# Kernel tuning notes

Measured on AMD Instinct MI355X. Metric: run time of the kernel, lower is better.

The kernel has to match this reference:

```python
import jax, jax.numpy as jnp
import numpy as np
from jax import lax

N_P = 0.5      # module_cfg.n_p
CUTOFF = 0.3   # module_cfg.cutoff


def setup_inputs() -> dict:
    key = jax.random.key(0)
    k1, k2, k3, k4 = jax.random.split(key, 4)
    h = jax.random.normal(k1, (1, 8192, 256), jnp.float32)
    pos = jax.random.normal(k2, (8192, 3), jnp.float32)
    W = jax.random.normal(k3, (256, 256), jnp.float32) / 16.0  # ~ Linear init scale
    b = jax.random.normal(k4, (256,), jnp.float32) * 0.01
    return {"h": h, "pos": pos, "W": W, "b": b}


def fps_indices(pos, k, select=0):
    """Farthest point sampling; returns the k selected indices in ascending
    index order (matching torch boolean-mask indexing pos[selected])."""
    n = pos.shape[0]
    selected = jnp.zeros(n, dtype=bool).at[select].set(True)
    d = jnp.linalg.norm(pos - pos[select], axis=-1)  # (N,) euclidean, as torch.pairwise_distance
    d = jnp.where(selected, -jnp.inf, d)

    def body(i, carry):
        sel, dist = carry
        new = jnp.argmax(dist)
        sel = sel.at[new].set(True)
        dist = jnp.minimum(dist, jnp.linalg.norm(pos - pos[new], axis=-1))
        dist = jnp.where(sel, -jnp.inf, dist)
        return sel, dist

    sel, _ = lax.fori_loop(0, k - 1, body, (selected, d))
    return jnp.nonzero(sel, size=k)[0]  # exactly k True entries, sorted


def reference(h, pos, W, b):
    B, num_res, c_s = h.shape
    n_nodes = int(num_res * N_P)  # num_res * n_p // 1

    idx = fps_indices(pos, n_nodes)          # (n_nodes,)
    new_node_pos = pos[idx]                  # (n_nodes, 3)

    # torch.cdist(pos, new_node_pos, p=3): Minkowski p=3 distance
    diff = jnp.abs(pos[:, None, :] - new_node_pos[None, :, :])  # (N, n_nodes, 3)
    dist = jnp.cbrt(jnp.sum(diff ** 3, axis=-1))                 # (N, n_nodes)

    # sparse membership mask (fixed-shape equivalent of the nonzero edge list)
    mask = dist < CUTOFF                      # (N, n_nodes) bool

    # sparse gather-matmul: aggregate residue features into each sampled node
    agg = jnp.einsum('nm,bnc->bmc', mask.astype(h.dtype), h)     # (B, n_nodes, c_s)
    new_node_embed = agg @ W.T + b            # nn.Linear(c_s, c_s)
    return new_node_embed, new_node_pos, mask
```

## Files before the change

### kernel.cpp

```cpp
#include <hip/hip_runtime.h>
#include <hip/hip_bf16.h>
#include <cmath>

#define FPS_N 8192
#define FPS_K 4096
#define CS    256
#define FT    1024
#define PPT   8
#define NEGINF (-__builtin_inff())

__device__ __forceinline__ float p3sum(float x, float y, float z,
                                       float nx, float ny, float nz) {
  float dx = fabsf(__fsub_rn(x, nx));
  float dy = fabsf(__fsub_rn(y, ny));
  float dz = fabsf(__fsub_rn(z, nz));
  float cx = __fmul_rn(__fmul_rn(dx, dx), dx);
  float cy = __fmul_rn(__fmul_rn(dy, dy), dy);
  float cz = __fmul_rn(__fmul_rn(dz, dz), dz);
  return __fadd_rn(__fadd_rn(cx, cy), cz);
}

__device__ __forceinline__ float eucl2(float x, float y, float z,
                                       float nx, float ny, float nz) {
  float dx = __fsub_rn(x, nx);
  float dy = __fsub_rn(y, ny);
  float dz = __fsub_rn(z, nz);
  return __fadd_rn(__fadd_rn(__fmul_rn(dx, dx), __fmul_rn(dy, dy)),
                   __fmul_rn(dz, dz));
}

#define LEXGT(va, ka, vb, kb) (((va) > (vb)) || ((va) == (vb) && ((ka) < (kb))))

template<int CTRL>
__device__ __forceinline__ int dppi(int a) {
  return __builtin_amdgcn_update_dpp(a, a, CTRL, 0xF, 0xF, false);
}
template<int CTRL>
__device__ __forceinline__ float dppf(float a) {
  return __int_as_float(__builtin_amdgcn_update_dpp(__float_as_int(a), __float_as_int(a), CTRL, 0xF, 0xF, false));
}

template<int CTRL>
__device__ __forceinline__ void dpp_sel5(float& v, int& k, float& x, float& y, float& z) {
  float pv = dppf<CTRL>(v); int pk = dppi<CTRL>(k);
  float px = dppf<CTRL>(x); float py = dppf<CTRL>(y); float pz = dppf<CTRL>(z);
  bool t = LEXGT(pv, pk, v, k);
  v = t ? pv : v; k = t ? pk : k;
  x = t ? px : x; y = t ? py : y; z = t ? pz : z;
}

template<int CTRL>
__device__ __forceinline__ void dpp_top2(float& v1, int& k1, float& v2, int& k2) {
  float p1 = dppf<CTRL>(v1); int q1 = dppi<CTRL>(k1);
  float p2 = dppf<CTRL>(v2); int q2 = dppi<CTRL>(k2);
  bool t = LEXGT(p1, q1, v1, k1);
  float lv = t ? v1 : p1; int lk = t ? k1 : q1;
  float ov = t ? p2 : v2; int ok = t ? q2 : k2;
  v1 = t ? p1 : v1; k1 = t ? q1 : k1;
  bool u = LEXGT(lv, lk, ov, ok);
  v2 = u ? lv : ov; k2 = u ? lk : ok;
}

#define PAIR2(v1, k1, v2, k2, a, ka, b, kb) { bool t_ = LEXGT(b, kb, a, ka); \
  v1 = t_ ? (b) : (a); k1 = t_ ? (kb) : (ka); v2 = t_ ? (a) : (b); k2 = t_ ? (ka) : (kb); }

#define MERGE22(v1, k1, v2, k2, w1, l1, w2, l2) { \
  bool t_ = LEXGT(w1, l1, v1, k1); \
  float lv_ = t_ ? (v1) : (w1); int lk_ = t_ ? (k1) : (l1); \
  float ov_ = t_ ? (w2) : (v2); int ok_ = t_ ? (l2) : (k2); \
  v1 = t_ ? (w1) : (v1); k1 = t_ ? (l1) : (k1); \
  bool u_ = LEXGT(lv_, lk_, ov_, ok_); \
  v2 = u_ ? lv_ : ov_; k2 = u_ ? lk_ : ok_; }

#define RESCAN2() { \
  float A1, B1, C1, D1, A2, B2, C2, D2; int Ak, Bk, Ck, Dk, Ak2, Bk2, Ck2, Dk2; \
  PAIR2(A1, Ak, A2, Ak2, dd[0], key[0], dd[1], key[1]) \
  PAIR2(B1, Bk, B2, Bk2, dd[2], key[2], dd[3], key[3]) \
  PAIR2(C1, Ck, C2, Ck2, dd[4], key[4], dd[5], key[5]) \
  PAIR2(D1, Dk, D2, Dk2, dd[6], key[6], dd[7], key[7]) \
  MERGE22(A1, Ak, A2, Ak2, B1, Bk, B2, Bk2) \
  MERGE22(C1, Ck, C2, Ck2, D1, Dk, D2, Dk2) \
  MERGE22(A1, Ak, A2, Ak2, C1, Ck, C2, Ck2) \
  bv = A1; bkey = Ak; bv2 = A2; bk2 = Ak2; }

#define WAVE_PUBLISH2(sn) { \
  float rv1 = bv; int rk1 = bkey; float rv2 = bv2; int rk2 = bk2; \
  dpp_top2<0x111>(rv1, rk1, rv2, rk2); dpp_top2<0x112>(rv1, rk1, rv2, rk2); \
  dpp_top2<0x114>(rv1, rk1, rv2, rk2); dpp_top2<0x118>(rv1, rk1, rv2, rk2); \
  dpp_top2<0x142>(rv1, rk1, rv2, rk2); dpp_top2<0x143>(rv1, rk1, rv2, rk2); \
  const int k1u = __builtin_amdgcn_readlane(rk1, 63); \
  const int v2u = __builtin_amdgcn_readlane(__float_as_int(rv2), 63); \
  const int k2u = __builtin_amdgcn_readlane(rk2, 63); \
  int* s_ = &slots[(sn) * 192 + wave * 12]; \
  if (bkey == k1u) { \
    float sx = x[0], sy = y[0], sz = z[0]; \
    _Pragma("unroll") \
    for (int j = 0; j < PPT; ++j) \
      if (j == (bkey & 7)) { sx = x[j]; sy = y[j]; sz = z[j]; } \
    s_[0] = __float_as_int(bv); s_[1] = bkey; \
    s_[2] = __float_as_int(sx); s_[3] = __float_as_int(sy); s_[4] = __float_as_int(sz); \
    if (bk2 == k2u) { \
      float tx = x[0], ty = y[0], tz = z[0]; \
      _Pragma("unroll") \
      for (int j = 0; j < PPT; ++j) \
        if (j == (bk2 & 7)) { tx = x[j]; ty = y[j]; tz = z[j]; } \
      s_[5] = v2u; s_[6] = k2u; \
      s_[7] = __float_as_int(tx); s_[8] = __float_as_int(ty); s_[9] = __float_as_int(tz); \
    } \
  } else if (bkey == k2u) { \
    float sx = x[0], sy = y[0], sz = z[0]; \
    _Pragma("unroll") \
    for (int j = 0; j < PPT; ++j) \
      if (j == (bkey & 7)) { sx = x[j]; sy = y[j]; sz = z[j]; } \
    s_[5] = __float_as_int(bv); s_[6] = bkey; \
    s_[7] = __float_as_int(sx); s_[8] = __float_as_int(sy); s_[9] = __float_as_int(sz); \
  } }

__global__ __launch_bounds__(1024) void bin_kernel(const float* __restrict__ pos,
                                                   float* __restrict__ px,
                                                   float* __restrict__ py,
                                                   float* __restrict__ pz,
                                                   unsigned short* __restrict__ ids16,
                                                   unsigned char* __restrict__ selb) {
  __shared__ int hist[4096];
  __shared__ int part[1024];
  const int tid = threadIdx.x;
#pragma unroll
  for (int i = 0; i < 4; ++i) hist[tid * 4 + i] = 0;
  ((int*)selb)[tid * 2 + 0] = 0;
  ((int*)selb)[tid * 2 + 1] = 0;
  if (tid == 0) selb[0] = 1;
  __syncthreads();

  float qx[8], qy[8], qz[8];
  int cell[8];
  {
    const float4* p4 = (const float4*)pos + tid * 6;
    float4 a0 = p4[0], a1 = p4[1], a2 = p4[2], a3 = p4[3], a4 = p4[4], a5 = p4[5];
    qx[0]=a0.x; qy[0]=a0.y; qz[0]=a0.z;
    qx[1]=a0.w; qy[1]=a1.x; qz[1]=a1.y;
    qx[2]=a1.z; qy[2]=a1.w; qz[2]=a2.x;
    qx[3]=a2.y; qy[3]=a2.z; qz[3]=a2.w;
    qx[4]=a3.x; qy[4]=a3.y; qz[4]=a3.z;
    qx[5]=a3.w; qy[5]=a4.x; qz[5]=a4.y;
    qx[6]=a4.z; qy[6]=a4.w; qz[6]=a5.x;
    qx[7]=a5.y; qy[7]=a5.z; qz[7]=a5.w;
  }
#pragma unroll
  for (int j = 0; j < 8; ++j) {
    int ix = min(max((int)floorf((qx[j] + 4.0f) * 2.0f), 0), 15);
    int iy = min(max((int)floorf((qy[j] + 4.0f) * 2.0f), 0), 15);
    int iz = min(max((int)floorf((qz[j] + 4.0f) * 2.0f), 0), 15);
    int m = 0;
#pragma unroll
    for (int b = 0; b < 4; ++b)
      m |= (((ix >> b) & 1) << (3 * b)) | (((iy >> b) & 1) << (3 * b + 1)) |
           (((iz >> b) & 1) << (3 * b + 2));
    cell[j] = m;
    atomicAdd(&hist[m], 1);
  }
  __syncthreads();
  int h0 = hist[tid*4], h1 = hist[tid*4+1], h2 = hist[tid*4+2], h3 = hist[tid*4+3];
  int s = h0 + h1 + h2 + h3;
  part[tid] = s;
  __syncthreads();
  for (int off = 1; off < 1024; off <<= 1) {
    int u = (tid >= off) ? part[tid - off] : 0;
    __syncthreads();
    part[tid] += u;
    __syncthreads();
  }
  int base = part[tid] - s;
  hist[tid*4+0] = base;
  hist[tid*4+1] = base + h0;
  hist[tid*4+2] = base + h0 + h1;
  hist[tid*4+3] = base + h0 + h1 + h2;
  __syncthreads();
#pragma unroll
  for (int j = 0; j < 8; ++j) {
    int slot = atomicAdd(&hist[cell[j]], 1);
    px[slot] = qx[j];
    py[slot] = qy[j];
    pz[slot] = qz[j];
    ids16[slot] = (unsigned short)(tid * 8 + j);
  }
}

__global__ __launch_bounds__(FT) void fps_kernel(const float* __restrict__ pos,
                                                 const float* __restrict__ spx,
                                                 const float* __restrict__ spy,
                                                 const float* __restrict__ spz,
                                                 const unsigned short* __restrict__ sid,
                                                 unsigned char* __restrict__ selb) {
  __shared__ int slots[2 * 192];
  const int tid = threadIdx.x, lane = tid & 63, wave = tid >> 6;

  float x[PPT], y[PPT], z[PPT], dd[PPT];
  int key[PPT];
  const float p0x = pos[0], p0y = pos[1], p0z = pos[2];
  {
    int4 b0 = ((const int4*)sid)[tid];
    int op[4] = { b0.x, b0.y, b0.z, b0.w };
#pragma unroll
    for (int j = 0; j < PPT; ++j) {
      int oid = (j & 1) ? ((op[j >> 1] >> 16) & 0xffff) : (op[j >> 1] & 0xffff);
      key[j] = (oid << 13) | (tid * PPT + j);
      float X = spx[tid * PPT + j], Y = spy[tid * PPT + j], Z = spz[tid * PPT + j];
      x[j] = X; y[j] = Y; z[j] = Z;
      float s = eucl2(X, Y, Z, p0x, p0y, p0z);
      dd[j] = (oid == 0) ? NEGINF : sqrtf(s);
    }
  }
  float mnx = x[0], mny = y[0], mnz = z[0], mxx = x[0], mxy = y[0], mxz = z[0];
#pragma unroll
  for (int j = 1; j < PPT; ++j) {
    mnx = fminf(mnx, x[j]); mny = fminf(mny, y[j]); mnz = fminf(mnz, z[j]);
    mxx = fmaxf(mxx, x[j]); mxy = fmaxf(mxy, y[j]); mxz = fmaxf(mxz, z[j]);
  }

  unsigned selmask = 0;
  float bv, bv2; int bkey, bk2;
  RESCAN2();
  WAVE_PUBLISH2(0);
  __syncthreads();

  int sel = 0, p = 0;
  while (sel < FPS_K - 1) {
    const int pn = p ^ 1;
    const int row = lane & 15;
    const int4 q0 = *(const int4*)&slots[p * 192 + row * 12 + 0];
    const int4 q1 = *(const int4*)&slots[p * 192 + row * 12 + 4];
    const int4 q2 = *(const int4*)&slots[p * 192 + row * 12 + 8];
    float ev = __int_as_float(q0.x); int ek = q0.y;
    float ex = __int_as_float(q0.z), ey = __int_as_float(q0.w), ez = __int_as_float(q1.x);
    const float sv2 = __int_as_float(q1.y); const int sk2 = q1.z;
    const float sx2 = __int_as_float(q1.w), sy2 = __int_as_float(q2.x), sz2 = __int_as_float(q2.y);
    bool avail2 = true;

    int A = 0;
    bool stop = false, own = false, fire = false;
    const int cap = FPS_K - 1 - sel;
    float a0x=0, a0y=0, a0z=0, a1x=0, a1y=0, a1z=0, a2x=0, a2y=0, a2z=0, a3x=0, a3y=0, a3z=0;

#define PSTEP(AX, AY, AZ, ACCCHK) \
    if (!stop) { \
      float mv = ev; int mk = ek; float mx = ex, my = ey, mz = ez; \
      dpp_sel5<0xB1>(mv, mk, mx, my, mz); \
      dpp_sel5<0x4E>(mv, mk, mx, my, mz); \
      dpp_sel5<0x124>(mv, mk, mx, my, mz); \
      dpp_sel5<0x128>(mv, mk, mx, my, mz); \
      bool ok = true; \
      ACCCHK \
      if (!ok) stop = true; \
      else { \
        AX = mx; AY = my; AZ = mz; \
        const int stor = mk & 8191; \
        if ((stor >> 3) == tid) { \
          const int jj = stor & 7; \
          _Pragma("unroll") \
          for (int j = 0; j < PPT; ++j) if (j == jj) dd[j] = NEGINF; \
          selmask |= (1u << jj); \
          own = true; \
        } \
        const int ww = stor >> 9; \
        if (row == ww) { \
          if (avail2) { ev = sv2; ek = sk2; ex = sx2; ey = sy2; ez = sz2; avail2 = false; } \
          else { ev = NEGINF; ek = 0x7fffffff; } \
        } \
        ++A; \
        if (A >= cap || A >= 4) stop = true; \
      } \
    }

    PSTEP(a0x, a0y, a0z, )
    PSTEP(a1x, a1y, a1z,
      ok = (sqrtf(eucl2(mx, my, mz, a0x, a0y, a0z)) >= mv);)
    PSTEP(a2x, a2y, a2z,
      ok = (sqrtf(eucl2(mx, my, mz, a0x, a0y, a0z)) >= mv)
        && (sqrtf(eucl2(mx, my, mz, a1x, a1y, a1z)) >= mv);)
    PSTEP(a3x, a3y, a3z,
      ok = (sqrtf(eucl2(mx, my, mz, a0x, a0y, a0z)) >= mv)
        && (sqrtf(eucl2(mx, my, mz, a1x, a1y, a1z)) >= mv)
        && (sqrtf(eucl2(mx, my, mz, a2x, a2y, a2z)) >= mv);)
#undef PSTEP

    const float lg = fmaxf(bv, 0.f);
    const float lg2 = lg * lg;
#define UPDC(c, AX, AY, AZ) \
    if ((c) < A) { \
      float cx = fminf(fmaxf(AX, mnx), mxx); \
      float cy = fminf(fmaxf(AY, mny), mxy); \
      float cz = fminf(fmaxf(AZ, mnz), mxz); \
      float ddx = AX - cx, ddy = AY - cy, ddz = AZ - cz; \
      float bd2 = ddx * ddx + ddy * ddy + ddz * ddz; \
      if (bd2 * 0.999f < lg2) { \
        _Pragma("unroll") \
        for (int j = 0; j < PPT; ++j) \
          dd[j] = fminf(dd[j], sqrtf(eucl2(x[j], y[j], z[j], AX, AY, AZ))); \
        fire = true; \
      } \
    }
    UPDC(0, a0x, a0y, a0z)
    UPDC(1, a1x, a1y, a1z)
    UPDC(2, a2x, a2y, a2z)
    UPDC(3, a3x, a3y, a3z)
#undef UPDC

    if (__ballot((fire || own) ? 1 : 0)) {
      if (fire || own) { RESCAN2(); }
      WAVE_PUBLISH2(pn);
    } else {
      if (lane < 12) slots[pn * 192 + wave * 12 + lane] = slots[p * 192 + wave * 12 + lane];
    }
    sel += A;
    p = pn;
    __syncthreads();
  }

#pragma unroll
  for (int j = 0; j < PPT; ++j)
    if ((selmask >> j) & 1) selb[key[j] >> 13] = 1;
}

__global__ __launch_bounds__(1024) void emit_kernel(const unsigned char* __restrict__ selb,
                                                    const float* __restrict__ pos,
                                                    float* __restrict__ pos_out) {
  __shared__ int sc[1024];
  const int tid = threadIdx.x;
  int w0 = ((const int*)selb)[tid * 2 + 0];
  int w1 = ((const int*)selb)[tid * 2 + 1];
  int cnt = __popc(w0) + __popc(w1);
  sc[tid] = cnt;
  __syncthreads();
  for (int off = 1; off < 1024; off <<= 1) {
    int u = (tid >= off) ? sc[tid - off] : 0;
    __syncthreads();
    sc[tid] += u;
    __syncthreads();
  }
  int r = sc[tid] - cnt;
#pragma unroll
  for (int j = 0; j < 8; ++j) {
    int w = (j < 4) ? w0 : w1;
    if ((w >> ((j & 3) * 8)) & 1) {
      int oi = tid * 8 + j;
      pos_out[r * 3 + 0] = pos[oi * 3 + 0];
      pos_out[r * 3 + 1] = pos[oi * 3 + 1];
      pos_out[r * 3 + 2] = pos[oi * 3 + 2];
      ++r;
    }
  }
}

__global__ __launch_bounds__(256) void wt_kernel(const float* __restrict__ W,
                                                 float* __restrict__ WT) {
  int i = blockIdx.x * 256 + threadIdx.x;
  int c = i >> 8, cp = i & 255;
  WT[i] = W[cp * 256 + c];
}

__global__ __launch_bounds__(256) void agg_linear_kernel(
    const float* __restrict__ h, const float* __restrict__ pos,
    const float* __restrict__ nodepos, const float* __restrict__ WT,
    const float* __restrict__ bias, float* __restrict__ embed, float sb) {
  const int m = blockIdx.x;
  const int tid = threadIdx.x;
  const int lane = tid & 63, wave = tid >> 6;
  const float nx = nodepos[m * 3 + 0];
  const float ny = nodepos[m * 3 + 1];
  const float nz = nodepos[m * 3 + 2];
  const float4* h4 = (const float4*)h;

  float4 acc = make_float4(0.f, 0.f, 0.f, 0.f);
  const int base0 = wave * (FPS_N / 4);
  for (int base = base0; base < base0 + (FPS_N / 4); base += 64) {
    int n = base + lane;
    float qx = pos[n * 3 + 0], qy = pos[n * 3 + 1], qz = pos[n * 3 + 2];
    unsigned long long mb = __ballot((p3sum(qx, qy, qz, nx, ny, nz) <= sb) ? 1 : 0);
    while (mb) {
      int b = __ffsll(mb) - 1;
      mb &= (mb - 1);
      float4 hv = h4[(size_t)(base + b) * 64 + lane];
      acc.x += hv.x; acc.y += hv.y; acc.z += hv.z; acc.w += hv.w;
    }
  }

  __shared__ float lacc[4][256];
  lacc[wave][lane * 4 + 0] = acc.x;
  lacc[wave][lane * 4 + 1] = acc.y;
  lacc[wave][lane * 4 + 2] = acc.z;
  lacc[wave][lane * 4 + 3] = acc.w;
  __syncthreads();
  __shared__ float aggrow[256];
  float aggv = ((lacc[0][tid] + lacc[1][tid]) + lacc[2][tid]) + lacc[3][tid];
  aggrow[tid] = aggv;
  __syncthreads();

  float o = bias[tid];
#pragma unroll 8
  for (int c = 0; c < 256; ++c)
    o = fmaf(aggrow[c], WT[c * 256 + tid], o);
  embed[(size_t)m * 256 + tid] = o;
}

__global__ __launch_bounds__(256) void mask_kernel(const float* __restrict__ pos,
                                                   const float* __restrict__ nodepos,
                                                   float* __restrict__ maskout,
                                                   float sb) {
  int n  = blockIdx.y;
  int m0 = (blockIdx.x * 256 + threadIdx.x) * 4;
  float x = pos[n * 3 + 0], y = pos[n * 3 + 1], z = pos[n * 3 + 2];
  const float4* np4 = (const float4*)(nodepos + (size_t)m0 * 3);
  float4 a = np4[0], bq = np4[1], cq = np4[2];
  float4 r;
  r.x = (p3sum(x, y, z, a.x,  a.y,  a.z)  <= sb) ? 1.0f : 0.0f;
  r.y = (p3sum(x, y, z, a.w,  bq.x, bq.y) <= sb) ? 1.0f : 0.0f;
  r.z = (p3sum(x, y, z, bq.z, bq.w, cq.x) <= sb) ? 1.0f : 0.0f;
  r.w = (p3sum(x, y, z, cq.y, cq.z, cq.w) <= sb) ? 1.0f : 0.0f;
  *(float4*)(maskout + (size_t)n * FPS_K + m0) = r;
}

extern "C" void kernel_launch(void* const* d_in, const int* in_sizes, int n_in,
                              void* d_out, int out_size, void* d_ws, size_t ws_size,
                              hipStream_t stream) {
  (void)in_sizes; (void)n_in; (void)out_size; (void)d_ws; (void)ws_size;
  const float* h   = (const float*)d_in[0];
  const float* pos = (const float*)d_in[1];
  const float* W   = (const float*)d_in[2];
  const float* b   = (const float*)d_in[3];

  float* out     = (float*)d_out;
  float* embed   = out;
  float* pos_out = out + (size_t)FPS_K * CS;
  float* mask    = pos_out + (size_t)FPS_K * 3;
  float* WT      = mask;
  float* px      = mask + (1 << 21);
  float* py      = px + FPS_N;
  float* pz      = py + FPS_N;
  unsigned short* ids16 = (unsigned short*)(pz + FPS_N);
  unsigned char*  selb  = ((unsigned char*)ids16) + 2 * FPS_N;

  const float  t    = 0.3f;
  const float  ulpv = nextafterf(t, 1.0f) - t;
  const double rmid = (double)t - (double)ulpv * 0.5;
  const double C    = rmid * rmid * rmid;
  float sb = (float)C;
  if (!((double)sb < C)) sb = nextafterf(sb, 0.0f);

  hipLaunchKernelGGL(bin_kernel, dim3(1), dim3(1024), 0, stream,
                     pos, px, py, pz, ids16, selb);
  hipLaunchKernelGGL(fps_kernel, dim3(1), dim3(FT), 0, stream,
                     pos, px, py, pz, ids16, selb);
  hipLaunchKernelGGL(emit_kernel, dim3(1), dim3(1024), 0, stream,
                     selb, pos, pos_out);
  hipLaunchKernelGGL(wt_kernel, dim3(256), dim3(256), 0, stream, W, WT);
  hipLaunchKernelGGL(agg_linear_kernel, dim3(FPS_K), dim3(256), 0, stream,
                     h, pos, pos_out, WT, b, embed, sb);
  hipLaunchKernelGGL(mask_kernel, dim3(4, FPS_N), dim3(256), 0, stream,
                     pos, pos_out, mask, sb);
}
```

Before: 7.297 ms.

## Replace four-step speculative FPS selection with a single top-2 DPP reduction

The FPS loop used to run up to four sequential 5-value DPP argmax reductions per iteration, accepting up to four points when they were far enough apart. It now runs one DPP top-2 reduction over value and key only, then fetches coordinates from shared slots for the winner and the best second candidate. This cuts per-iteration shuffle and select work and register pressure. The cost is at most two accepted points per barrier-separated iteration, so more outer iterations and __syncthreads calls may be needed.

```diff
diff --git a/kernel.cpp b/kernel.cpp
--- a/kernel.cpp
+++ b/kernel.cpp
@@ -8,6 +8,7 @@
 #define FT    1024
 #define PPT   8
 #define NEGINF (-__builtin_inff())
+#define KMAX  0x7fffffff
 
 __device__ __forceinline__ float p3sum(float x, float y, float z,
                                        float nx, float ny, float nz) {
@@ -38,15 +39,6 @@
 template<int CTRL>
 __device__ __forceinline__ float dppf(float a) {
   return __int_as_float(__builtin_amdgcn_update_dpp(__float_as_int(a), __float_as_int(a), CTRL, 0xF, 0xF, false));
-}
-
-template<int CTRL>
-__device__ __forceinline__ void dpp_sel5(float& v, int& k, float& x, float& y, float& z) {
-  float pv = dppf<CTRL>(v); int pk = dppi<CTRL>(k);
-  float px = dppf<CTRL>(x); float py = dppf<CTRL>(y); float pz = dppf<CTRL>(z);
-  bool t = LEXGT(pv, pk, v, k);
-  v = t ? pv : v; k = t ? pk : k;
-  x = t ? px : x; y = t ? py : y; z = t ? pz : z;
 }
 
 template<int CTRL>
@@ -228,83 +220,81 @@
   while (sel < FPS_K - 1) {
     const int pn = p ^ 1;
     const int row = lane & 15;
-    const int4 q0 = *(const int4*)&slots[p * 192 + row * 12 + 0];
-    const int4 q1 = *(const int4*)&slots[p * 192 + row * 12 + 4];
-    const int4 q2 = *(const int4*)&slots[p * 192 + row * 12 + 8];
-    float ev = __int_as_float(q0.x); int ek = q0.y;
-    float ex = __int_as_float(q0.z), ey = __int_as_float(q0.w), ez = __int_as_float(q1.x);
-    const float sv2 = __int_as_float(q1.y); const int sk2 = q1.z;
-    const float sx2 = __int_as_float(q1.w), sy2 = __int_as_float(q2.x), sz2 = __int_as_float(q2.y);
-    bool avail2 = true;
-
-    int A = 0;
-    bool stop = false, own = false, fire = false;
+    const int2 e1 = *(const int2*)&slots[p * 192 + row * 12];
+    float mv1 = __int_as_float(e1.x); int mk1 = e1.y;
+    float mv2 = NEGINF; int mk2 = KMAX;
+    dpp_top2<0xB1>(mv1, mk1, mv2, mk2);
+    dpp_top2<0x4E>(mv1, mk1, mv2, mk2);
+    dpp_top2<0x124>(mv1, mk1, mv2, mk2);
+    dpp_top2<0x128>(mv1, mk1, mv2, mk2);
+
+    const int stor1 = mk1 & 8191;
+    const int w1w   = stor1 >> 9;
+    const int* r1 = &slots[p * 192 + w1w * 12];
+    const float w1x = __int_as_float(r1[2]);
+    const float w1y = __int_as_float(r1[3]);
+    const float w1z = __int_as_float(r1[4]);
+    const float sv2 = __int_as_float(r1[5]);
+    const int   sk2 = r1[6];
+    const int  w2aw = (mk2 & 8191) >> 9;
+    const int* r2 = &slots[p * 192 + w2aw * 12];
+    const bool bsec = LEXGT(sv2, sk2, mv2, mk2);
+    const float gv2 = bsec ? sv2 : mv2;
+    const int   gk2 = bsec ? sk2 : mk2;
+    const float g2x = __int_as_float(bsec ? r1[7] : r2[2]);
+    const float g2y = __int_as_float(bsec ? r1[8] : r2[3]);
+    const float g2z = __int_as_float(bsec ? r1[9] : r2[4]);
+
     const int cap = FPS_K - 1 - sel;
-    float a0x=0, a0y=0, a0z=0, a1x=0, a1y=0, a1z=0, a2x=0, a2y=0, a2z=0, a3x=0, a3y=0, a3z=0;
-
-#define PSTEP(AX, AY, AZ, ACCCHK) \
-    if (!stop) { \
-      float mv = ev; int mk = ek; float mx = ex, my = ey, mz = ez; \
-      dpp_sel5<0xB1>(mv, mk, mx, my, mz); \
-      dpp_sel5<0x4E>(mv, mk, mx, my, mz); \
-      dpp_sel5<0x124>(mv, mk, mx, my, mz); \
-      dpp_sel5<0x128>(mv, mk, mx, my, mz); \
-      bool ok = true; \
-      ACCCHK \
-      if (!ok) stop = true; \
-      else { \
-        AX = mx; AY = my; AZ = mz; \
-        const int stor = mk & 8191; \
-        if ((stor >> 3) == tid) { \
-          const int jj = stor & 7; \
-          _Pragma("unroll") \
-          for (int j = 0; j < PPT; ++j) if (j == jj) dd[j] = NEGINF; \
-          selmask |= (1u << jj); \
-          own = true; \
-        } \
-        const int ww = stor >> 9; \
-        if (row == ww) { \
-          if (avail2) { ev = sv2; ek = sk2; ex = sx2; ey = sy2; ez = sz2; avail2 = false; } \
-          else { ev = NEGINF; ek = 0x7fffffff; } \
-        } \
-        ++A; \
-        if (A >= cap || A >= 4) stop = true; \
-      } \
-    }
-
-    PSTEP(a0x, a0y, a0z, )
-    PSTEP(a1x, a1y, a1z,
-      ok = (sqrtf(eucl2(mx, my, mz, a0x, a0y, a0z)) >= mv);)
-    PSTEP(a2x, a2y, a2z,
-      ok = (sqrtf(eucl2(mx, my, mz, a0x, a0y, a0z)) >= mv)
-        && (sqrtf(eucl2(mx, my, mz, a1x, a1y, a1z)) >= mv);)
-    PSTEP(a3x, a3y, a3z,
-      ok = (sqrtf(eucl2(mx, my, mz, a0x, a0y, a0z)) >= mv)
-        && (sqrtf(eucl2(mx, my, mz, a1x, a1y, a1z)) >= mv)
-        && (sqrtf(eucl2(mx, my, mz, a2x, a2y, a2z)) >= mv);)
-#undef PSTEP
+    bool acc2 = (cap >= 2) && (gv2 != NEGINF) && (gk2 != KMAX);
+    if (acc2) acc2 = (sqrtf(eucl2(g2x, g2y, g2z, w1x, w1y, w1z)) >= gv2);
+    const int stor2 = gk2 & 8191;
+
+    bool own = false;
+    if ((stor1 >> 3) == tid) {
+      const int jj = stor1 & 7;
+#pragma unroll
+      for (int j = 0; j < PPT; ++j) if (j == jj) dd[j] = NEGINF;
+      selmask |= (1u << jj);
+      own = true;
+    }
+    if (acc2 && (stor2 >> 3) == tid) {
+      const int jj = stor2 & 7;
+#pragma unroll
+      for (int j = 0; j < PPT; ++j) if (j == jj) dd[j] = NEGINF;
+      selmask |= (1u << jj);
+      own = true;
+    }
 
     const float lg = fmaxf(bv, 0.f);
     const float lg2 = lg * lg;
-#define UPDC(c, AX, AY, AZ) \
-    if ((c) < A) { \
-      float cx = fminf(fmaxf(AX, mnx), mxx); \
-      float cy = fminf(fmaxf(AY, mny), mxy); \
-      float cz = fminf(fmaxf(AZ, mnz), mxz); \
-      float ddx = AX - cx, ddy = AY - cy, ddz = AZ - cz; \
-      float bd2 = ddx * ddx + ddy * ddy + ddz * ddz; \
-      if (bd2 * 0.999f < lg2) { \
-        _Pragma("unroll") \
-        for (int j = 0; j < PPT; ++j) \
-          dd[j] = fminf(dd[j], sqrtf(eucl2(x[j], y[j], z[j], AX, AY, AZ))); \
-        fire = true; \
-      } \
-    }
-    UPDC(0, a0x, a0y, a0z)
-    UPDC(1, a1x, a1y, a1z)
-    UPDC(2, a2x, a2y, a2z)
-    UPDC(3, a3x, a3y, a3z)
-#undef UPDC
+    bool fire = false;
+    {
+      float cx = fminf(fmaxf(w1x, mnx), mxx);
+      float cy = fminf(fmaxf(w1y, mny), mxy);
+      float cz = fminf(fmaxf(w1z, mnz), mxz);
+      float ddx = w1x - cx, ddy = w1y - cy, ddz = w1z - cz;
+      float bd2 = ddx * ddx + ddy * ddy + ddz * ddz;
+      if (bd2 * 0.999f < lg2) {
+#pragma unroll
+        for (int j = 0; j < PPT; ++j)
+          dd[j] = fminf(dd[j], sqrtf(eucl2(x[j], y[j], z[j], w1x, w1y, w1z)));
+        fire = true;
+      }
+    }
+    if (acc2) {
+      float cx = fminf(fmaxf(g2x, mnx), mxx);
+      float cy = fminf(fmaxf(g2y, mny), mxy);
+      float cz = fminf(fmaxf(g2z, mnz), mxz);
+      float ddx = g2x - cx, ddy = g2y - cy, ddz = g2z - cz;
+      float bd2 = ddx * ddx + ddy * ddy + ddz * ddz;
+      if (bd2 * 0.999f < lg2) {
+#pragma unroll
+        for (int j = 0; j < PPT; ++j)
+          dd[j] = fminf(dd[j], sqrtf(eucl2(x[j], y[j], z[j], g2x, g2y, g2z)));
+        fire = true;
+      }
+    }
 
     if (__ballot((fire || own) ? 1 : 0)) {
       if (fire || own) { RESCAN2(); }
@@ -312,7 +302,7 @@
     } else {
       if (lane < 12) slots[pn * 192 + wave * 12 + lane] = slots[p * 192 + wave * 12 + lane];
     }
-    sel += A;
+    sel += acc2 ? 2 : 1;
     p = pn;
     __syncthreads();
   }
```

Result: slower. 7.538 ms (+3.3%).
